# Kernel tuning notes

Hardware: AMD Instinct MI355X
Metric: run time of the kernel (lower is better)

Reference implementation:

```python
import jax, jax.numpy as jnp
import numpy as np
from jax import lax

# dims: B=batch, T=seq_len, D=inputSize, H=hiddenSize, L=num_layers, N=3 cell nodes
B, T, D, H, L = 128, 64, 256, 256, 2
WSCALE = 0.05  # scale on randn weight init for numerical health (math unchanged)


def setup_inputs() -> dict:
    key = jax.random.key(0)
    ks = jax.random.split(key, 8)
    return {
        "x": jax.random.normal(ks[0], (B, T, D), dtype=jnp.float32),
        "hidden": jax.random.normal(ks[1], (L, B, H), dtype=jnp.float32),
        # per-timestep cell parameters (the torch module instantiates one cell per timestep)
        "Win0": jax.random.normal(ks[2], (T, D, H), dtype=jnp.float32) * WSCALE,
        "Wh0": jax.random.normal(ks[3], (T, 3, H, H), dtype=jnp.float32) * WSCALE,
        "b0": jax.random.normal(ks[4], (T, 3, H), dtype=jnp.float32) * WSCALE,
        "Win1": jax.random.normal(ks[5], (T, H, H), dtype=jnp.float32) * WSCALE,
        "Wh1": jax.random.normal(ks[6], (T, 3, H, H), dtype=jnp.float32) * WSCALE,
        "b1": jax.random.normal(ks[7], (T, 3, H), dtype=jnp.float32) * WSCALE,
    }


def _cell(xt, h, Win, Wh, b):
    # cellList=[0,0,1,0,2]: activations [tanh, relu, sigmoid], connections [0, 0]
    n0 = jnp.tanh(xt @ Win + h @ Wh[0] + b[0])          # node 0
    n1 = jax.nn.relu(n0 @ Wh[1] + b[1]) + n0            # node 1 (+ node 0 via connection)
    n2 = jax.nn.sigmoid(n1 @ Wh[2] + b[2]) + n0         # node 2 (+ node 0 via connection)
    # unconnected nodes = {1, 2} -> mean over their values
    return 0.5 * (n1 + n2)


def _run_layer(xs_tbd, h0, Win, Wh, b):
    def step(h, inp):
        xt, Wi, Whh, bt = inp
        hn = _cell(xt, h, Wi, Whh, bt)
        return hn, hn
    h_last, outs = lax.scan(step, h0, (xs_tbd, Win, Wh, b))
    return outs, h_last  # outs: [T,B,H]


def reference(x, hidden, Win0, Wh0, b0, Win1, Wh1, b1):
    x_t = jnp.transpose(x, (1, 0, 2))                    # [T,B,D] (batch_first input)
    out0, h0f = _run_layer(x_t, hidden[0], Win0, Wh0, b0)
    out1, h1f = _run_layer(out0, hidden[1], Win1, Wh1, b1)
    output = jnp.transpose(out1, (1, 0, 2))              # [B,T,H], batch_first
    hidden_out = jnp.stack([h0f, h1f], axis=0)           # [L,B,H]
    return output, hidden_out
```

## Files before the change

kernel.cpp:

```cpp
#include <hip/hip_runtime.h>


typedef _Float16 f16;
typedef __attribute__((ext_vector_type(8))) _Float16 f16x8;
typedef __attribute__((ext_vector_type(4))) float f32x4;
typedef __attribute__((ext_vector_type(4))) float float4v;

#define Tt 64
#define FLAG_MAGIC 0x52570000

#define WS_WH0T   0
#define WS_WIN1T  25165824
#define WS_WH1T   33554432
#define WS_WIN0T  58720256
#define WS_XW     67108864
#define WS_HSEQ   75497472
#define WS_FLAGS  79691776

__device__ __forceinline__ void sb() { __builtin_amdgcn_sched_barrier(0); }

template <int N>
__device__ __forceinline__ void waitvm() {
  __builtin_amdgcn_s_waitcnt(0x0F70 | (N & 15) | ((N >> 4) << 14));
}
__device__ __forceinline__ void waitlgkm0() { __builtin_amdgcn_s_waitcnt(0xC07F); }

__device__ __forceinline__ void barx() {
  asm volatile("s_waitcnt lgkmcnt(0)\n\ts_barrier" ::: "memory");
}

__device__ __forceinline__ void dma16(const void* g, void* l) {
  __builtin_amdgcn_global_load_lds(
      (const __attribute__((address_space(1))) unsigned int*)g,
      (__attribute__((address_space(3))) unsigned int*)l, 16, 0, 0);
}

__device__ __forceinline__ float tanh_fast(float x) {
  float xc = fminf(fmaxf(x, -15.f), 15.f);
  float e = __expf(2.f * xc);
  return (e - 1.f) / (e + 1.f);
}
__device__ __forceinline__ float sigmoid_fast(float x) { return 1.f / (1.f + __expf(-x)); }

__global__ __launch_bounds__(256) void transpose_cvt_kernel(
    const float* __restrict__ Wh0, const float* __restrict__ Win1,
    const float* __restrict__ Wh1, const float* __restrict__ Win0,
    f16* __restrict__ Wh0T, f16* __restrict__ Win1T, f16* __restrict__ Wh1T,
    f16* __restrict__ Win0T) {
  __shared__ float tile[256 * 33];
  const int bid = blockIdx.x;
  const int mat = bid >> 3, n0 = (bid & 7) << 5;
  const float* src; f16* dst;
  if (mat < 192)      { src = Wh0  + (size_t)mat * 65536;         dst = Wh0T  + (size_t)mat * 65536; }
  else if (mat < 256) { src = Win1 + (size_t)(mat - 192) * 65536; dst = Win1T + (size_t)(mat - 192) * 65536; }
  else if (mat < 448) { src = Wh1  + (size_t)(mat - 256) * 65536; dst = Wh1T  + (size_t)(mat - 256) * 65536; }
  else                { src = Win0 + (size_t)(mat - 448) * 65536; dst = Win0T + (size_t)(mat - 448) * 65536; }
  const int tid = threadIdx.x;
  const int c2 = tid & 15, kl = tid >> 4;
#pragma unroll
  for (int p = 0; p < 16; ++p) {
    const int k = kl + p * 16;
    float2 v = *(const float2*)(src + k * 256 + n0 + c2 * 2);
    tile[k * 33 + c2 * 2]     = v.x;
    tile[k * 33 + c2 * 2 + 1] = v.y;
  }
  __syncthreads();
  const int n = tid & 7, c = tid >> 3;
#pragma unroll
  for (int it = 0; it < 4; ++it) {
    const int nn = n + it * 8;
    f16x8 vv;
#pragma unroll
    for (int i = 0; i < 8; ++i) vv[i] = (f16)tile[(c * 8 + i) * 33 + nn];
    *(f16x8*)((char*)dst + (size_t)(n0 + nn) * 512 + c * 16) = vv;
  }
}

__global__ __launch_bounds__(512, 2) void xw_kernel(
    const float* __restrict__ x, const f16* __restrict__ Win0T,
    const float* __restrict__ b0, float* __restrict__ xw) {
  const int t = blockIdx.x >> 3, bb = blockIdx.x & 7;
  const int rb = bb << 4;
  const int tid = threadIdx.x, lane = tid & 63, w = tid >> 6;
  const int q = lane >> 4, mn = lane & 15, dr = q * 4;
  const f16* wt = Win0T + (size_t)t * 65536;
  const float4v* xr = (const float4v*)(x + ((size_t)(rb + mn) * Tt + t) * 256);
  f32x4 acc[2] = {{0.f,0.f,0.f,0.f},{0.f,0.f,0.f,0.f}};
#pragma unroll
  for (int kt = 0; kt < 8; ++kt) {
    const int k0 = kt * 32 + q * 8;
    float4v x0 = xr[k0 / 4], x1 = xr[k0 / 4 + 1];
    f16x8 a = {(f16)x0.x, (f16)x0.y, (f16)x0.z, (f16)x0.w,
               (f16)x1.x, (f16)x1.y, (f16)x1.z, (f16)x1.w};
#pragma unroll
    for (int nt = 0; nt < 2; ++nt) {
      f16x8 b = *(const f16x8*)(wt + (size_t)(w * 32 + nt * 16 + mn) * 256 + k0);
      acc[nt] = __builtin_amdgcn_mfma_f32_16x16x32_f16(a, b, acc[nt], 0, 0, 0);
    }
  }
#pragma unroll
  for (int nt = 0; nt < 2; ++nt) {
    const int n = w * 32 + nt * 16 + mn;
    const float bv = b0[(size_t)t * 768 + n];
#pragma unroll
    for (int r = 0; r < 4; ++r)
      xw[(size_t)t * 32768 + (size_t)(rb + dr + r) * 256 + n] = acc[nt][r] + bv;
  }
}

template <int NW, bool DMA>
__device__ __forceinline__ void phase(f32x4 (&acc)[2], const char* arow, const char* wb,
                                      const int (&bo)[4], const char* gnext, char* lnext,
                                      const int (&off)[8], int q) {
  waitvm<NW>();
  sb();
  f16x8 a[4], b[8];
#pragma unroll
  for (int kt = 0; kt < 4; ++kt) {
    a[kt]         = *(const f16x8*)(arow + kt * 64 + q * 16);
    b[kt * 2]     = *(const f16x8*)(wb + bo[kt]);
    b[kt * 2 + 1] = *(const f16x8*)(wb + bo[kt] + 4096);
  }
  sb();
  waitlgkm0();
  if (DMA) {
#pragma unroll
    for (int d = 0; d < 8; ++d) dma16(gnext + off[d], lnext + d * 1024);
  }
  sb();
#pragma unroll
  for (int kt = 0; kt < 4; ++kt) {
    acc[0] = __builtin_amdgcn_mfma_f32_16x16x32_f16(a[kt], b[kt * 2],     acc[0], 0, 0, 0);
    acc[1] = __builtin_amdgcn_mfma_f32_16x16x32_f16(a[kt], b[kt * 2 + 1], acc[1], 0, 0, 0);
  }
}

template <int NW>
__device__ __forceinline__ void phaseRA(f32x4 (&acc)[2], const f16x8* af, const char* wb,
                                        const int (&bo)[4], const char* gnext, char* lnext,
                                        const int (&off)[8]) {
  waitvm<NW>();
  sb();
  f16x8 b[8];
#pragma unroll
  for (int kt = 0; kt < 4; ++kt) {
    b[kt * 2]     = *(const f16x8*)(wb + bo[kt]);
    b[kt * 2 + 1] = *(const f16x8*)(wb + bo[kt] + 4096);
  }
  sb();
  waitlgkm0();
#pragma unroll
  for (int d = 0; d < 8; ++d) dma16(gnext + off[d], lnext + d * 1024);
  sb();
#pragma unroll
  for (int kt = 0; kt < 4; ++kt) {
    acc[0] = __builtin_amdgcn_mfma_f32_16x16x32_f16(af[kt], b[kt * 2],     acc[0], 0, 0, 0);
    acc[1] = __builtin_amdgcn_mfma_f32_16x16x32_f16(af[kt], b[kt * 2 + 1], acc[1], 0, 0, 0);
  }
}

__global__ __launch_bounds__(512, 1) void rnn_kernel(
    const float* __restrict__ hidden,
    const f16* __restrict__ Wh0T, const float* __restrict__ b0,
    const f16* __restrict__ Win1T, const f16* __restrict__ Wh1T, const float* __restrict__ b1,
    const float* __restrict__ xw, f16* __restrict__ hseq, int* __restrict__ flags,
    float* __restrict__ out) {
  __shared__ __align__(16) char smem[147968];
  char* wlds = smem;
  char* abuf = smem + 131072;
  char* nbuf = smem + 139520;

  const int xcd = blockIdx.x & 7, slot = blockIdx.x >> 3;
  bool isL0; int g;
  if (xcd < 2)                  { isL0 = true;  g = xcd * 4 + slot; }
  else if (xcd >= 4 && xcd < 6) { isL0 = false; g = (xcd - 4) * 4 + slot; }
  else return;

  const int tid = threadIdx.x;
  const int lane = tid & 63;
  const int w = tid >> 6;
  const int q = lane >> 4;
  const int mn = lane & 15;
  const int rb = g << 4;
  const int nc = w * 32 + mn;
  const int dr = q * 4;
  const int wslice = w * 16384;

  int off[8], bo[4];
#pragma unroll
  for (int d = 0; d < 8; ++d) {
    const int row = 4 * d + q;
    off[d] = row * 512 + ((mn ^ (row & 15)) << 4);
  }
#pragma unroll
  for (int kt = 0; kt < 4; ++kt)
    bo[kt] = mn * 256 + (((kt * 4 + q) ^ mn) << 4);

  const float* hsrc = hidden + (isL0 ? 0 : 32768) + (size_t)rb * 256;
  for (int i = tid; i < 16 * 256; i += 512) {
    const int m = i >> 8, n = i & 255;
    *(f16*)(abuf + m * 528 + n * 2) = (f16)hsrc[m * 256 + n];
  }

  char* bufA = wlds + wslice;
  char* bufB = bufA + 8192;
  const f32x4 zero4 = {0.f, 0.f, 0.f, 0.f};
  float n0v[2][4], n1v[2][4];

  if (isL0) {
    const char* WB = (const char*)Wh0T;
    {
      const char* gw = WB + wslice;
#pragma unroll
      for (int d = 0; d < 8; ++d) dma16(gw + off[d], bufA + d * 1024);
#pragma unroll
      for (int d = 0; d < 8; ++d) dma16(gw + 256 + off[d], bufB + d * 1024);
      sb();
    }
    barx();

#pragma unroll 1
    for (int t = 0; t < Tt; ++t) {
      const int tn = (t < Tt - 1) ? t + 1 : t;
      const bool last = (t == Tt - 1);
      const char* wt  = WB + (size_t)t * 393216 + wslice;
      const char* wtn = WB + (size_t)tn * 393216 + wslice;

      float xwv[2][4];
#pragma unroll
      for (int nt = 0; nt < 2; ++nt)
#pragma unroll
        for (int r = 0; r < 4; ++r)
          xwv[nt][r] = xw[(size_t)t * 32768 + (size_t)(rb + dr + r) * 256 + nc + nt * 16];
      const float bv1a = b0[(size_t)t * 768 + 256 + nc], bv1b = b0[(size_t)t * 768 + 256 + nc + 16];
      const float bv2a = b0[(size_t)t * 768 + 512 + nc], bv2b = b0[(size_t)t * 768 + 512 + nc + 16];
      sb();

      f32x4 acc[2];
      acc[0] = zero4; acc[1] = zero4;
      phase<20, true>(acc, abuf + mn * 528,       bufA, bo, wt + 131072,       bufA, off, q);
      phase<20, true>(acc, abuf + mn * 528 + 256, bufB, bo, wt + 131072 + 256, bufB, off, q);
      waitvm<20>();
      sb();
#pragma unroll
      for (int nt = 0; nt < 2; ++nt)
#pragma unroll
        for (int r = 0; r < 4; ++r) {
          float v = tanh_fast(acc[nt][r] + xwv[nt][r]);
          n0v[nt][r] = v;
          *(f16*)(nbuf + (dr + r) * 528 + (nc + nt * 16) * 2) = (f16)v;
        }
      barx();

      acc[0] = zero4; acc[1] = zero4;
      phase<8, true>(acc, nbuf + mn * 528,       bufA, bo, wt + 262144,       bufA, off, q);
      phase<8, true>(acc, nbuf + mn * 528 + 256, bufB, bo, wt + 262144 + 256, bufB, off, q);
      barx();
#pragma unroll
      for (int nt = 0; nt < 2; ++nt) {
        const float bv = nt ? bv1b : bv1a;
#pragma unroll
        for (int r = 0; r < 4; ++r) {
          float v = fmaxf(acc[nt][r] + bv, 0.f) + n0v[nt][r];
          n1v[nt][r] = v;
          *(f16*)(nbuf + (dr + r) * 528 + (nc + nt * 16) * 2) = (f16)v;
        }
      }
      barx();

      acc[0] = zero4; acc[1] = zero4;
      phase<8, false>(acc, nbuf + mn * 528,       bufA, bo, wt, bufA, off, q);
      phase<0, false>(acc, nbuf + mn * 528 + 256, bufB, bo, wt, bufB, off, q);
#pragma unroll
      for (int nt = 0; nt < 2; ++nt) {
        const float bv = nt ? bv2b : bv2a;
#pragma unroll
        for (int r = 0; r < 4; ++r) {
          float s = sigmoid_fast(acc[nt][r] + bv);
          float hv = 0.5f * (n1v[nt][r] + s + n0v[nt][r]);
          f16 h16 = (f16)hv;
          *(f16*)(abuf + (dr + r) * 528 + (nc + nt * 16) * 2) = h16;
          hseq[((size_t)(g * 64 + t)) * 4096 + (dr + r) * 256 + nc + nt * 16] = h16;
          if (last) out[2097152 + (size_t)(rb + dr + r) * 256 + nc + nt * 16] = hv;
        }
      }
      waitvm<0>();
      __threadfence();
      __syncthreads();
      if (tid == 0) {
        __hip_atomic_store(&flags[g * 64 + t], FLAG_MAGIC | (t + 1),
                           __ATOMIC_RELEASE, __HIP_MEMORY_SCOPE_AGENT);
      }
      sb();
      {
        const char* gw = wtn;
#pragma unroll
        for (int d = 0; d < 8; ++d) dma16(gw + off[d], bufA + d * 1024);
#pragma unroll
        for (int d = 0; d < 8; ++d) dma16(gw + 256 + off[d], bufB + d * 1024);
        sb();
      }
    }
  } else {
    const char* WI = (const char*)Win1T;
    const char* WH = (const char*)Wh1T;
    const f16* hsg = hseq + (size_t)g * 64 * 4096;
    {
      const char* gw = WH + wslice;
#pragma unroll
      for (int d = 0; d < 8; ++d) dma16(gw + off[d], bufA + d * 1024);
#pragma unroll
      for (int d = 0; d < 8; ++d) dma16(gw + 256 + off[d], bufB + d * 1024);
      sb();
    }
    barx();

#pragma unroll 1
    for (int t = 0; t < Tt; ++t) {
      const int tn = (t < Tt - 1) ? t + 1 : t;
      const bool last = (t == Tt - 1);
      const char* wit = WI + (size_t)t * 131072 + wslice;
      const char* wht = WH + (size_t)t * 393216 + wslice;
      const char* whn = WH + (size_t)tn * 393216 + wslice;

      {
        const int want = FLAG_MAGIC | (t + 1);
        while (__hip_atomic_load(&flags[g * 64 + t], __ATOMIC_ACQUIRE,
                                 __HIP_MEMORY_SCOPE_AGENT) != want) {}
      }
      sb();
      const char* ht = (const char*)(hsg + (size_t)t * 4096);
      f16x8 af[8];
#pragma unroll
      for (int kt = 0; kt < 8; ++kt)
        af[kt] = *(const f16x8*)(ht + mn * 512 + kt * 64 + q * 16);
      const float bv0a = b1[(size_t)t * 768 + nc],       bv0b = b1[(size_t)t * 768 + nc + 16];
      const float bv1a = b1[(size_t)t * 768 + 256 + nc], bv1b = b1[(size_t)t * 768 + 256 + nc + 16];
      const float bv2a = b1[(size_t)t * 768 + 512 + nc], bv2b = b1[(size_t)t * 768 + 512 + nc + 16];
      sb();

      f32x4 acc[2];
      acc[0] = zero4; acc[1] = zero4;
      phase<63, true>(acc, abuf + mn * 528,       bufA, bo, wit,       bufA, off, q);
      phase<63, true>(acc, abuf + mn * 528 + 256, bufB, bo, wit + 256, bufB, off, q);
      phaseRA<8>(acc, af,     bufA, bo, wht + 131072,       bufA, off);
      phaseRA<8>(acc, af + 4, bufB, bo, wht + 131072 + 256, bufB, off);
#pragma unroll
      for (int nt = 0; nt < 2; ++nt) {
        const float bv = nt ? bv0b : bv0a;
#pragma unroll
        for (int r = 0; r < 4; ++r) {
          float v = tanh_fast(acc[nt][r] + bv);
          n0v[nt][r] = v;
          *(f16*)(nbuf + (dr + r) * 528 + (nc + nt * 16) * 2) = (f16)v;
        }
      }
      barx();

      acc[0] = zero4; acc[1] = zero4;
      phase<8, true>(acc, nbuf + mn * 528,       bufA, bo, wht + 262144,       bufA, off, q);
      phase<8, true>(acc, nbuf + mn * 528 + 256, bufB, bo, wht + 262144 + 256, bufB, off, q);
      barx();
#pragma unroll
      for (int nt = 0; nt < 2; ++nt) {
        const float bv = nt ? bv1b : bv1a;
#pragma unroll
        for (int r = 0; r < 4; ++r) {
          float v = fmaxf(acc[nt][r] + bv, 0.f) + n0v[nt][r];
          n1v[nt][r] = v;
          *(f16*)(nbuf + (dr + r) * 528 + (nc + nt * 16) * 2) = (f16)v;
        }
      }
      barx();

      acc[0] = zero4; acc[1] = zero4;
      phase<8, true>(acc, nbuf + mn * 528,       bufA, bo, whn,       bufA, off, q);
      phase<8, true>(acc, nbuf + mn * 528 + 256, bufB, bo, whn + 256, bufB, off, q);
#pragma unroll
      for (int nt = 0; nt < 2; ++nt) {
        const float bv = nt ? bv2b : bv2a;
#pragma unroll
        for (int r = 0; r < 4; ++r) {
          float s = sigmoid_fast(acc[nt][r] + bv);
          float hv = 0.5f * (n1v[nt][r] + s + n0v[nt][r]);
          *(f16*)(abuf + (dr + r) * 528 + (nc + nt * 16) * 2) = (f16)hv;
          out[((size_t)(rb + dr + r) * Tt + t) * 256 + nc + nt * 16] = hv;
          if (last) out[2097152 + 32768 + (size_t)(rb + dr + r) * 256 + nc + nt * 16] = hv;
        }
      }
      barx();
    }
  }
}

extern "C" void kernel_launch(void* const* d_in, const int* in_sizes, int n_in,
                              void* d_out, int out_size, void* d_ws, size_t ws_size,
                              hipStream_t stream) {
  (void)in_sizes; (void)n_in; (void)out_size; (void)ws_size;
  const float* x      = (const float*)d_in[0];
  const float* hidden = (const float*)d_in[1];
  const float* Win0   = (const float*)d_in[2];
  const float* Wh0    = (const float*)d_in[3];
  const float* b0     = (const float*)d_in[4];
  const float* Win1   = (const float*)d_in[5];
  const float* Wh1    = (const float*)d_in[6];
  const float* b1     = (const float*)d_in[7];
  float* out = (float*)d_out;

  char* ws = (char*)d_ws;
  f16* Wh0T  = (f16*)(ws + WS_WH0T);
  f16* Win1T = (f16*)(ws + WS_WIN1T);
  f16* Wh1T  = (f16*)(ws + WS_WH1T);
  f16* Win0T = (f16*)(ws + WS_WIN0T);
  float* xwp = (float*)(ws + WS_XW);
  f16* hseq  = (f16*)(ws + WS_HSEQ);
  int* flags = (int*)(ws + WS_FLAGS);

  transpose_cvt_kernel<<<dim3(4096), dim3(256), 0, stream>>>(
      Wh0, Win1, Wh1, Win0, Wh0T, Win1T, Wh1T, Win0T);
  xw_kernel<<<dim3(512), dim3(512), 0, stream>>>(x, Win0T, b0, xwp);
  rnn_kernel<<<dim3(32), dim3(512), 0, stream>>>(
      hidden, Wh0T, b0, Win1T, Wh1T, b1, xwp, hseq, flags, out);
}
```

Measured before the change: 854.7 us.

## Move layer-1 input projection into layer-0 blocks to shorten layer-1 critical path

Layer-0 blocks now also compute h0_t @ Win1[t] + b1[0] right after producing h0_t and write the fp32 pre-activation to a workspace sequence. Layer-1 blocks no longer do that GEMM after waiting on the flag. They can issue their recurrent h @ Wh1[0] GEMM before waiting, which takes the input-projection work off the layer-1 dependency chain. The grid shrinks from 32 blocks with XCD-based mapping to 16 contiguous blocks, and the transpose kernel's thread-to-element mapping for the write phase is changed. The cost is an extra GEMM per step on the layer-0 chain and a larger fp32 handoff buffer in place of the fp16 one.

```diff
diff --git a/kernel.cpp b/kernel.cpp
--- a/kernel.cpp
+++ b/kernel.cpp
@@ -14,8 +14,8 @@
 #define WS_WH1T   33554432
 #define WS_WIN0T  58720256
 #define WS_XW     67108864
-#define WS_HSEQ   75497472
-#define WS_FLAGS  79691776
+#define WS_P3     75497472
+#define WS_FLAGS  83886080
 
 __device__ __forceinline__ void sb() { __builtin_amdgcn_sched_barrier(0); }
 
@@ -65,7 +65,7 @@
     tile[k * 33 + c2 * 2 + 1] = v.y;
   }
   __syncthreads();
-  const int n = tid & 7, c = tid >> 3;
+  const int n = tid >> 5, c = tid & 31;
 #pragma unroll
   for (int it = 0; it < 4; ++it) {
     const int nn = n + it * 8;
@@ -135,52 +135,24 @@
   }
 }
 
-template <int NW>
-__device__ __forceinline__ void phaseRA(f32x4 (&acc)[2], const f16x8* af, const char* wb,
-                                        const int (&bo)[4], const char* gnext, char* lnext,
-                                        const int (&off)[8]) {
-  waitvm<NW>();
-  sb();
-  f16x8 b[8];
-#pragma unroll
-  for (int kt = 0; kt < 4; ++kt) {
-    b[kt * 2]     = *(const f16x8*)(wb + bo[kt]);
-    b[kt * 2 + 1] = *(const f16x8*)(wb + bo[kt] + 4096);
-  }
-  sb();
-  waitlgkm0();
-#pragma unroll
-  for (int d = 0; d < 8; ++d) dma16(gnext + off[d], lnext + d * 1024);
-  sb();
-#pragma unroll
-  for (int kt = 0; kt < 4; ++kt) {
-    acc[0] = __builtin_amdgcn_mfma_f32_16x16x32_f16(af[kt], b[kt * 2],     acc[0], 0, 0, 0);
-    acc[1] = __builtin_amdgcn_mfma_f32_16x16x32_f16(af[kt], b[kt * 2 + 1], acc[1], 0, 0, 0);
-  }
-}
-
 __global__ __launch_bounds__(512, 1) void rnn_kernel(
     const float* __restrict__ hidden,
     const f16* __restrict__ Wh0T, const float* __restrict__ b0,
     const f16* __restrict__ Win1T, const f16* __restrict__ Wh1T, const float* __restrict__ b1,
-    const float* __restrict__ xw, f16* __restrict__ hseq, int* __restrict__ flags,
+    const float* __restrict__ xw, float* __restrict__ p3seq, int* __restrict__ flags,
     float* __restrict__ out) {
   __shared__ __align__(16) char smem[147968];
   char* wlds = smem;
   char* abuf = smem + 131072;
   char* nbuf = smem + 139520;
 
-  const int xcd = blockIdx.x & 7, slot = blockIdx.x >> 3;
-  bool isL0; int g;
-  if (xcd < 2)                  { isL0 = true;  g = xcd * 4 + slot; }
-  else if (xcd >= 4 && xcd < 6) { isL0 = false; g = (xcd - 4) * 4 + slot; }
-  else return;
-
   const int tid = threadIdx.x;
   const int lane = tid & 63;
   const int w = tid >> 6;
   const int q = lane >> 4;
   const int mn = lane & 15;
+  const bool isL0 = blockIdx.x < 8;
+  const int g = blockIdx.x & 7;
   const int rb = g << 4;
   const int nc = w * 32 + mn;
   const int dr = q * 4;
@@ -209,6 +181,7 @@
 
   if (isL0) {
     const char* WB = (const char*)Wh0T;
+    const char* WI = (const char*)Win1T;
     {
       const char* gw = WB + wslice;
 #pragma unroll
@@ -225,6 +198,7 @@
       const bool last = (t == Tt - 1);
       const char* wt  = WB + (size_t)t * 393216 + wslice;
       const char* wtn = WB + (size_t)tn * 393216 + wslice;
+      const char* wit = WI + (size_t)t * 131072 + wslice;
 
       float xwv[2][4];
 #pragma unroll
@@ -234,13 +208,14 @@
           xwv[nt][r] = xw[(size_t)t * 32768 + (size_t)(rb + dr + r) * 256 + nc + nt * 16];
       const float bv1a = b0[(size_t)t * 768 + 256 + nc], bv1b = b0[(size_t)t * 768 + 256 + nc + 16];
       const float bv2a = b0[(size_t)t * 768 + 512 + nc], bv2b = b0[(size_t)t * 768 + 512 + nc + 16];
+      const float p3ba = b1[(size_t)t * 768 + nc],       p3bb = b1[(size_t)t * 768 + nc + 16];
       sb();
 
       f32x4 acc[2];
       acc[0] = zero4; acc[1] = zero4;
-      phase<20, true>(acc, abuf + mn * 528,       bufA, bo, wt + 131072,       bufA, off, q);
-      phase<20, true>(acc, abuf + mn * 528 + 256, bufB, bo, wt + 131072 + 256, bufB, off, q);
-      waitvm<20>();
+      phase<22, true>(acc, abuf + mn * 528,       bufA, bo, wt + 131072,       bufA, off, q);
+      phase<22, true>(acc, abuf + mn * 528 + 256, bufB, bo, wt + 131072 + 256, bufB, off, q);
+      waitvm<16>();
       sb();
 #pragma unroll
       for (int nt = 0; nt < 2; ++nt)
@@ -269,8 +244,8 @@
       barx();
 
       acc[0] = zero4; acc[1] = zero4;
-      phase<8, false>(acc, nbuf + mn * 528,       bufA, bo, wt, bufA, off, q);
-      phase<0, false>(acc, nbuf + mn * 528 + 256, bufB, bo, wt, bufB, off, q);
+      phase<8, true>(acc, nbuf + mn * 528,       bufA, bo, wit,       bufA, off, q);
+      phase<8, true>(acc, nbuf + mn * 528 + 256, bufB, bo, wit + 256, bufB, off, q);
 #pragma unroll
       for (int nt = 0; nt < 2; ++nt) {
         const float bv = nt ? bv2b : bv2a;
@@ -278,11 +253,22 @@
         for (int r = 0; r < 4; ++r) {
           float s = sigmoid_fast(acc[nt][r] + bv);
           float hv = 0.5f * (n1v[nt][r] + s + n0v[nt][r]);
-          f16 h16 = (f16)hv;
-          *(f16*)(abuf + (dr + r) * 528 + (nc + nt * 16) * 2) = h16;
-          hseq[((size_t)(g * 64 + t)) * 4096 + (dr + r) * 256 + nc + nt * 16] = h16;
+          *(f16*)(abuf + (dr + r) * 528 + (nc + nt * 16) * 2) = (f16)hv;
           if (last) out[2097152 + (size_t)(rb + dr + r) * 256 + nc + nt * 16] = hv;
         }
+      }
+      barx();
+
+      acc[0] = zero4; acc[1] = zero4;
+      phase<8, false>(acc, abuf + mn * 528,       bufA, bo, wt, bufA, off, q);
+      phase<0, false>(acc, abuf + mn * 528 + 256, bufB, bo, wt, bufB, off, q);
+#pragma unroll
+      for (int nt = 0; nt < 2; ++nt) {
+        const float bv = nt ? p3bb : p3ba;
+#pragma unroll
+        for (int r = 0; r < 4; ++r)
+          p3seq[(size_t)(g * 64 + t) * 4096 + (dr + r) * 256 + nc + nt * 16] =
+              acc[nt][r] + bv;
       }
       waitvm<0>();
       __threadfence();
@@ -302,9 +288,8 @@
       }
     }
   } else {
-    const char* WI = (const char*)Win1T;
     const char* WH = (const char*)Wh1T;
-    const f16* hsg = hseq + (size_t)g * 64 * 4096;
+    const float* p3g = p3seq + (size_t)g * 64 * 4096;
     {
       const char* gw = WH + wslice;
 #pragma unroll
@@ -312,6 +297,7 @@
 #pragma unroll
       for (int d = 0; d < 8; ++d) dma16(gw + 256 + off[d], bufB + d * 1024);
       sb();
+      waitvm<0>();
     }
     barx();
 
@@ -319,9 +305,13 @@
     for (int t = 0; t < Tt; ++t) {
       const int tn = (t < Tt - 1) ? t + 1 : t;
       const bool last = (t == Tt - 1);
-      const char* wit = WI + (size_t)t * 131072 + wslice;
       const char* wht = WH + (size_t)t * 393216 + wslice;
       const char* whn = WH + (size_t)tn * 393216 + wslice;
+
+      f32x4 acc[2];
+      acc[0] = zero4; acc[1] = zero4;
+      phase<17, true>(acc, abuf + mn * 528,       bufA, bo, wht + 131072,       bufA, off, q);
+      phase<9,  true>(acc, abuf + mn * 528 + 256, bufB, bo, wht + 131072 + 256, bufB, off, q);
 
       {
         const int want = FLAG_MAGIC | (t + 1);
@@ -329,37 +319,30 @@
                                  __HIP_MEMORY_SCOPE_AGENT) != want) {}
       }
       sb();
-      const char* ht = (const char*)(hsg + (size_t)t * 4096);
-      f16x8 af[8];
-#pragma unroll
-      for (int kt = 0; kt < 8; ++kt)
-        af[kt] = *(const f16x8*)(ht + mn * 512 + kt * 64 + q * 16);
-      const float bv0a = b1[(size_t)t * 768 + nc],       bv0b = b1[(size_t)t * 768 + nc + 16];
+      float p3v[2][4];
+#pragma unroll
+      for (int nt = 0; nt < 2; ++nt)
+#pragma unroll
+        for (int r = 0; r < 4; ++r)
+          p3v[nt][r] = p3g[(size_t)t * 4096 + (dr + r) * 256 + nc + nt * 16];
       const float bv1a = b1[(size_t)t * 768 + 256 + nc], bv1b = b1[(size_t)t * 768 + 256 + nc + 16];
       const float bv2a = b1[(size_t)t * 768 + 512 + nc], bv2b = b1[(size_t)t * 768 + 512 + nc + 16];
       sb();
-
-      f32x4 acc[2];
-      acc[0] = zero4; acc[1] = zero4;
-      phase<63, true>(acc, abuf + mn * 528,       bufA, bo, wit,       bufA, off, q);
-      phase<63, true>(acc, abuf + mn * 528 + 256, bufB, bo, wit + 256, bufB, off, q);
-      phaseRA<8>(acc, af,     bufA, bo, wht + 131072,       bufA, off);
-      phaseRA<8>(acc, af + 4, bufB, bo, wht + 131072 + 256, bufB, off);
-#pragma unroll
-      for (int nt = 0; nt < 2; ++nt) {
-        const float bv = nt ? bv0b : bv0a;
-#pragma unroll
-        for (int r = 0; r < 4; ++r) {
-          float v = tanh_fast(acc[nt][r] + bv);
+      waitvm<0>();
+      sb();
+#pragma unroll
+      for (int nt = 0; nt < 2; ++nt)
+#pragma unroll
+        for (int r = 0; r < 4; ++r) {
+          float v = tanh_fast(acc[nt][r] + p3v[nt][r]);
           n0v[nt][r] = v;
           *(f16*)(nbuf + (dr + r) * 528 + (nc + nt * 16) * 2) = (f16)v;
         }
-      }
-      barx();
-
-      acc[0] = zero4; acc[1] = zero4;
-      phase<8, true>(acc, nbuf + mn * 528,       bufA, bo, wht + 262144,       bufA, off, q);
-      phase<8, true>(acc, nbuf + mn * 528 + 256, bufB, bo, wht + 262144 + 256, bufB, off, q);
+      barx();
+
+      acc[0] = zero4; acc[1] = zero4;
+      phase<63, true>(acc, nbuf + mn * 528,       bufA, bo, wht + 262144,       bufA, off, q);
+      phase<63, true>(acc, nbuf + mn * 528 + 256, bufB, bo, wht + 262144 + 256, bufB, off, q);
       barx();
 #pragma unroll
       for (int nt = 0; nt < 2; ++nt) {
@@ -408,17 +391,17 @@
   float* out = (float*)d_out;
 
   char* ws = (char*)d_ws;
-  f16* Wh0T  = (f16*)(ws + WS_WH0T);
-  f16* Win1T = (f16*)(ws + WS_WIN1T);
-  f16* Wh1T  = (f16*)(ws + WS_WH1T);
-  f16* Win0T = (f16*)(ws + WS_WIN0T);
-  float* xwp = (float*)(ws + WS_XW);
-  f16* hseq  = (f16*)(ws + WS_HSEQ);
-  int* flags = (int*)(ws + WS_FLAGS);
+  f16* Wh0T   = (f16*)(ws + WS_WH0T);
+  f16* Win1T  = (f16*)(ws + WS_WIN1T);
+  f16* Wh1T   = (f16*)(ws + WS_WH1T);
+  f16* Win0T  = (f16*)(ws + WS_WIN0T);
+  float* xwp  = (float*)(ws + WS_XW);
+  float* p3p  = (float*)(ws + WS_P3);
+  int* flags  = (int*)(ws + WS_FLAGS);
 
   transpose_cvt_kernel<<<dim3(4096), dim3(256), 0, stream>>>(
       Wh0, Win1, Wh1, Win0, Wh0T, Win1T, Wh1T, Win0T);
   xw_kernel<<<dim3(512), dim3(512), 0, stream>>>(x, Win0T, b0, xwp);
-  rnn_kernel<<<dim3(32), dim3(512), 0, stream>>>(
-      hidden, Wh0T, b0, Win1T, Wh1T, b1, xwp, hseq, flags, out);
-}
+  rnn_kernel<<<dim3(16), dim3(512), 0, stream>>>(
+      hidden, Wh0T, b0, Win1T, Wh1T, b1, xwp, p3p, flags, out);
+}
```

Result: faster. 804.5 us (-5.9%).
